# Performance work log

Measured on AMD Instinct MI355X. Metric: run time of the kernel, lower is better.

The kernel has to match this reference:

```python
import jax, jax.numpy as jnp
import numpy as np

INF = 100000000.0
TOPK = 13
ALPHA = 1
BETA = 6


def box_cxcywh_to_xyxy(b):
    cx, cy, w, h = jnp.split(b, 4, axis=-1)
    return jnp.concatenate([cx - 0.5 * w, cy - 0.5 * h, cx + 0.5 * w, cy + 0.5 * h], axis=-1)


def generalized_box_iou(boxes1, boxes2):
    # boxes1: [N,4] xyxy, boxes2: [G,4] xyxy -> [N,G]
    area1 = (boxes1[:, 2] - boxes1[:, 0]) * (boxes1[:, 3] - boxes1[:, 1])
    area2 = (boxes2[:, 2] - boxes2[:, 0]) * (boxes2[:, 3] - boxes2[:, 1])
    lt = jnp.maximum(boxes1[:, None, :2], boxes2[None, :, :2])
    rb = jnp.minimum(boxes1[:, None, 2:], boxes2[None, :, 2:])
    wh = jnp.clip(rb - lt, 0.0)
    inter = wh[..., 0] * wh[..., 1]
    union = area1[:, None] + area2[None, :] - inter
    iou = inter / union
    lt_e = jnp.minimum(boxes1[:, None, :2], boxes2[None, :, :2])
    rb_e = jnp.maximum(boxes1[:, None, 2:], boxes2[None, :, 2:])
    wh_e = jnp.clip(rb_e - lt_e, 0.0)
    area_e = wh_e[..., 0] * wh_e[..., 1]
    return iou - (area_e - union) / area_e


def _assign_one(cls_logits, bbox_pred, gt_boxes, gt_labels):
    # cls_logits [N,C], bbox_pred [N,4] cxcywh, gt_boxes [G,4] cxcywh, gt_labels [G]
    N = bbox_pred.shape[0]
    G = gt_boxes.shape[0]
    scores = jax.nn.sigmoid(cls_logits)
    overlaps = -generalized_box_iou(box_cxcywh_to_xyxy(bbox_pred), box_cxcywh_to_xyxy(gt_boxes))  # [N,G]
    bbox_scores = scores[:, gt_labels]                       # [N,G] gather per-gt class score
    alignment = bbox_scores ** ALPHA * overlaps ** BETA      # [N,G]
    # per-gt topk over queries
    cand_metrics, cand_idxs = jax.lax.top_k(alignment.T, TOPK)  # [G,K]
    is_pos = cand_metrics > 0
    vals = jnp.take_along_axis(overlaps.T, cand_idxs, axis=1)   # [G,K]
    rows = jnp.broadcast_to(jnp.arange(G)[:, None], (G, TOPK))
    cols = jnp.where(is_pos, cand_idxs, N)  # out-of-bounds col -> dropped
    oinf = jnp.full((G, N), -INF, dtype=overlaps.dtype)
    oinf = oinf.at[rows, cols].set(vals, mode='drop')
    max_overlaps = oinf.max(axis=0)     # [N]
    argmax_overlaps = oinf.argmax(axis=0)
    pos = max_overlaps != -INF
    assigned_gt_inds = jnp.where(pos, argmax_overlaps + 1, 0)
    assign_metrics = jnp.where(pos, alignment[jnp.arange(N), argmax_overlaps], 0.0)
    assigned_labels = jnp.where(pos, gt_labels[argmax_overlaps], -1)
    return assigned_gt_inds, assigned_labels, assign_metrics


def setup_inputs() -> dict:
    key = jax.random.key(0)
    k1, k2, k3, k4 = jax.random.split(key, 4)
    bs, N, C, G = 16, 4000, 80, 300
    return {
        'pred_logits': jax.random.normal(k1, (bs, N, C), dtype=jnp.float32),
        'pred_boxes': jax.random.uniform(k2, (bs, N, 4), dtype=jnp.float32, minval=0.05, maxval=0.95),
        'gt_boxes': jax.random.uniform(k3, (bs, G, 4), dtype=jnp.float32, minval=0.05, maxval=0.95),
        'gt_labels': jax.random.randint(k4, (bs, G), 0, C),
    }


def reference(pred_logits, pred_boxes, gt_boxes, gt_labels):
    # Fixed-shape equivalent of matched_list: assigned_gt_inds[b,q] == 0 means
    # background; k>0 means query q matched to gt k-1 (same semantics as the
    # (valid_query_idx, valid_assigned_gt_inds) pairs in the torch code).
    return jax.vmap(_assign_one)(pred_logits, pred_boxes, gt_boxes, gt_labels)
```

## Files before the change

### kernel.cpp

```cpp
#include <hip/hip_runtime.h>

#define NPRED  4000
#define NGROUP 1000
#define NGT    300
#define NCLS   80
#define TOPKK  13
#define NCHUNK 125

typedef unsigned long long u64;

__device__ __forceinline__ float frcp(float x) { return __builtin_amdgcn_rcpf(x); }
__device__ __forceinline__ float fexp(float x) {
    return __builtin_amdgcn_exp2f(x * 1.44269504088896341f);
}

__device__ __forceinline__ float neg_giou_pa(float4 p, float pa, float gx1, float gy1,
                                             float gx2, float gy2, float garea) {
    float whx = fmaxf(fminf(p.z, gx2) - fmaxf(p.x, gx1), 0.0f);
    float why = fmaxf(fminf(p.w, gy2) - fmaxf(p.y, gy1), 0.0f);
    float inter = whx * why;
    float uni = pa + garea - inter;
    float iou = inter * frcp(uni);
    float wex = fmaxf(p.z, gx2) - fminf(p.x, gx1);
    float wey = fmaxf(p.w, gy2) - fminf(p.y, gy1);
    float area_e = wex * wey;
    return (area_e - uni) * frcp(area_e) - iou;
}

__device__ __forceinline__ float4 to_xyxy(float4 pb) {
    return make_float4(pb.x - 0.5f * pb.z, pb.y - 0.5f * pb.w,
                       pb.x + 0.5f * pb.z, pb.y + 0.5f * pb.w);
}

__device__ __forceinline__ float sigmoid_fast(float x) {
    return frcp(1.0f + fexp(-x));
}

__device__ __forceinline__ float pow6(float x) {
    float x2 = x * x;
    float x4 = x2 * x2;
    return x2 * x4;
}

__device__ __forceinline__ unsigned ord_float(float f) {
    unsigned u = __float_as_uint(f);
    return u ^ ((unsigned)(((int)u) >> 31) | 0x80000000u);
}

__device__ __forceinline__ u64 pack_key(float v, int n) {
    return ((u64)__float_as_uint(v) << 32) | (u64)(~(unsigned)n);
}

__device__ __forceinline__ u64 wave_max_key(u64 b1) {
    float fv = __uint_as_float((unsigned)(b1 >> 32));
    float mv = fv;
    #pragma unroll
    for (int m = 1; m < 64; m <<= 1)
        mv = fmaxf(mv, __shfl_xor(mv, m, 64));
    u64 tied = __ballot(fv == mv);
    if ((tied & (tied - 1)) == 0ULL) {
        int src = __ffsll((unsigned long long)tied) - 1;
        return __shfl(b1, src, 64);
    }
    u64 t = b1;
    #pragma unroll
    for (int m = 1; m < 64; m <<= 1) {
        u64 o = __shfl_xor(t, m, 64);
        if (o > t) t = o;
    }
    return t;
}

__global__ void init_keys(u64* keys, int n) {
    int i = blockIdx.x * blockDim.x + threadIdx.x;
    if (i < n) keys[i] = 0ULL;
}

__global__ __launch_bounds__(256) void sig_transpose(const float* __restrict__ logits,
                                                     const float4* __restrict__ pboxes,
                                                     float* __restrict__ st,
                                                     float4* __restrict__ pxyxy,
                                                     float* __restrict__ parea,
                                                     u64* __restrict__ keys,
                                                     int total_keys) {
    const int tid = threadIdx.x;
    const int gid = blockIdx.x * 256 + tid;
    if (gid < total_keys) keys[gid] = 0ULL;

    const int b = blockIdx.x / NCHUNK;
    const int n0 = (blockIdx.x % NCHUNK) * 32;

    if (tid < 32) {
        int n = n0 + tid;
        float4 x = to_xyxy(pboxes[(size_t)b * NPRED + n]);
        pxyxy[(size_t)b * NPRED + n] = x;
        parea[(size_t)b * NPRED + n] = (x.z - x.x) * (x.w - x.y);
    }

    __shared__ float tile[NCLS][32 + 1];

    const float4* src = (const float4*)(logits + ((size_t)b * NPRED + n0) * NCLS);
    #pragma unroll
    for (int it = 0; it < 3; ++it) {
        int i4 = tid + it * 256;
        if (i4 < 640) {
            int p = i4 / 20;
            int c = (i4 - p * 20) * 4;
            float4 v = src[i4];
            tile[c + 0][p] = sigmoid_fast(v.x);
            tile[c + 1][p] = sigmoid_fast(v.y);
            tile[c + 2][p] = sigmoid_fast(v.z);
            tile[c + 3][p] = sigmoid_fast(v.w);
        }
    }
    __syncthreads();
    float* dstbase = st + (size_t)b * NCLS * NPRED + n0;
    #pragma unroll
    for (int it = 0; it < 3; ++it) {
        int w4 = tid + it * 256;
        if (w4 < 640) {
            int c = w4 >> 3, r4 = (w4 & 7) * 4;
            float4 v = make_float4(tile[c][r4], tile[c][r4 + 1],
                                   tile[c][r4 + 2], tile[c][r4 + 3]);
            *(float4*)(dstbase + (size_t)c * NPRED + r4) = v;
        }
    }
}

template <bool PRE>
__global__ __launch_bounds__(256) void topk_scatter(const float* __restrict__ logits,
                                                    const float* __restrict__ st,
                                                    const float4* __restrict__ pboxes,
                                                    const float4* __restrict__ pxyxy,
                                                    const float* __restrict__ parea,
                                                    const float4* __restrict__ gboxes,
                                                    const int* __restrict__ glabels,
                                                    u64* __restrict__ keys) {
    const int blk = blockIdx.x;
    const int b = blk / NGT;
    const int g = blk - b * NGT;
    const int tid = threadIdx.x;
    const int wave = tid >> 6;
    const int lane = tid & 63;

    __shared__ __align__(16) float s_key[NPRED];
    __shared__ u64 s_wave[4];
    __shared__ u64 s_win[TOPKK];

    float4 gb = gboxes[b * NGT + g];
    const int lab = glabels[b * NGT + g];
    const float gx1 = gb.x - 0.5f * gb.z;
    const float gy1 = gb.y - 0.5f * gb.w;
    const float gx2 = gb.x + 0.5f * gb.z;
    const float gy2 = gb.y + 0.5f * gb.w;
    const float garea = (gx2 - gx1) * (gy2 - gy1);

    const float* lg = logits + (size_t)b * NPRED * NCLS + lab;
    const float* srow = st + ((size_t)b * NCLS + lab) * NPRED;
    const float4* srow4 = (const float4*)srow;
    const float4* par4 = (const float4*)(parea + (size_t)b * NPRED);
    const float4* pbb = pboxes + (size_t)b * NPRED;
    const float4* pxr = pxyxy + (size_t)b * NPRED;

    float bv1 = -1.0f, bv2 = -1.0f;
    int   bn1 = 0,     bn2 = 0;
    #pragma unroll
    for (int j = 0; j < 4; ++j) {
        int grp = tid + j * 256;
        if (grp < NGROUP) {
            int n0 = grp * 4;
            float s0, s1, s2, s3;
            float4 p0, p1, p2, p3;
            float a0, a1, a2, a3;
            if (PRE) {
                float4 s4 = srow4[grp];
                s0 = s4.x; s1 = s4.y; s2 = s4.z; s3 = s4.w;
                float4 a4 = par4[grp];
                a0 = a4.x; a1 = a4.y; a2 = a4.z; a3 = a4.w;
                p0 = pxr[n0]; p1 = pxr[n0 + 1]; p2 = pxr[n0 + 2]; p3 = pxr[n0 + 3];
            } else {
                s0 = sigmoid_fast(lg[(size_t)(n0 + 0) * NCLS]);
                s1 = sigmoid_fast(lg[(size_t)(n0 + 1) * NCLS]);
                s2 = sigmoid_fast(lg[(size_t)(n0 + 2) * NCLS]);
                s3 = sigmoid_fast(lg[(size_t)(n0 + 3) * NCLS]);
                p0 = to_xyxy(pbb[n0]);     p1 = to_xyxy(pbb[n0 + 1]);
                p2 = to_xyxy(pbb[n0 + 2]); p3 = to_xyxy(pbb[n0 + 3]);
                a0 = (p0.z - p0.x) * (p0.w - p0.y);
                a1 = (p1.z - p1.x) * (p1.w - p1.y);
                a2 = (p2.z - p2.x) * (p2.w - p2.y);
                a3 = (p3.z - p3.x) * (p3.w - p3.y);
            }
            float v0 = s0 * pow6(neg_giou_pa(p0, a0, gx1, gy1, gx2, gy2, garea));
            float v1 = s1 * pow6(neg_giou_pa(p1, a1, gx1, gy1, gx2, gy2, garea));
            float v2 = s2 * pow6(neg_giou_pa(p2, a2, gx1, gy1, gx2, gy2, garea));
            float v3 = s3 * pow6(neg_giou_pa(p3, a3, gx1, gy1, gx2, gy2, garea));
            *(float4*)&s_key[n0] = make_float4(v0, v1, v2, v3);
            if (v0 > bv1) { bv2 = bv1; bn2 = bn1; bv1 = v0; bn1 = n0; }
            else if (v0 > bv2) { bv2 = v0; bn2 = n0; }
            if (v1 > bv1) { bv2 = bv1; bn2 = bn1; bv1 = v1; bn1 = n0 + 1; }
            else if (v1 > bv2) { bv2 = v1; bn2 = n0 + 1; }
            if (v2 > bv1) { bv2 = bv1; bn2 = bn1; bv1 = v2; bn1 = n0 + 2; }
            else if (v2 > bv2) { bv2 = v2; bn2 = n0 + 2; }
            if (v3 > bv1) { bv2 = bv1; bn2 = bn1; bv1 = v3; bn1 = n0 + 3; }
            else if (v3 > bv2) { bv2 = v3; bn2 = n0 + 3; }
        }
    }
    u64 b1 = pack_key(bv1, bn1);
    u64 b2 = pack_key(bv2, bn2);

    {
        u64 m1 = wave_max_key(b1);
        if (lane == 0) s_wave[wave] = m1;
    }

    int nwin = 0;
    for (int k = 0; k < TOPKK; ++k) {
        __syncthreads();
        u64 t1 = s_wave[0];
        u64 c;
        c = s_wave[1]; if (c > t1) t1 = c;
        c = s_wave[2]; if (c > t1) t1 = c;
        c = s_wave[3]; if (c > t1) t1 = c;
        if ((unsigned)(t1 >> 32) == 0u) break;
        if (tid == 0) s_win[k] = t1;
        nwin = k + 1;
        int n1 = (int)(~(unsigned)t1);
        int ownerTid = (n1 >> 2) & 255;
        if (tid == ownerTid) {
            s_key[n1] = 0.0f;
            if (b2 != 0ULL) { b1 = b2; b2 = 0ULL; }
            else {
                b1 = 0ULL;
                #pragma unroll
                for (int jj = 0; jj < 4; ++jj) {
                    int grp = tid + jj * 256;
                    if (grp >= NGROUP) continue;
                    int n0 = grp * 4;
                    float4 q = *(const float4*)&s_key[n0];
                    u64 c0 = pack_key(q.x, n0);
                    u64 c1 = pack_key(q.y, n0 + 1);
                    u64 c2 = pack_key(q.z, n0 + 2);
                    u64 c3 = pack_key(q.w, n0 + 3);
                    if (c0 > b1) { b2 = b1; b1 = c0; } else if (c0 > b2) b2 = c0;
                    if (c1 > b1) { b2 = b1; b1 = c1; } else if (c1 > b2) b2 = c1;
                    if (c2 > b1) { b2 = b1; b1 = c2; } else if (c2 > b2) b2 = c2;
                    if (c3 > b1) { b2 = b1; b1 = c3; } else if (c3 > b2) b2 = c3;
                }
            }
        }
        if ((ownerTid >> 6) == wave) {
            u64 m1 = wave_max_key(b1);
            if (lane == 0) s_wave[wave] = m1;
        }
    }
    __syncthreads();

    if (tid < nwin) {
        u64 t = s_win[tid];
        int wi = (int)(~(unsigned)t);
        float4 p;
        if (PRE) p = pxr[wi];
        else     p = to_xyxy(pbb[wi]);
        float pa = (p.z - p.x) * (p.w - p.y);
        float o = neg_giou_pa(p, pa, gx1, gy1, gx2, gy2, garea);
        unsigned mbits = (unsigned)(t >> 32) >> 16;
        u64 key = ((u64)ord_float(o) << 32)
                | ((u64)(511u - (unsigned)g) << 23)
                | ((u64)mbits << 7);
        atomicMax(&keys[(size_t)b * NPRED + wi], key);
    }
}

__global__ void finalize(const int* __restrict__ glabels,
                         const u64* __restrict__ keys,
                         float* __restrict__ out, int total) {
    int i = blockIdx.x * blockDim.x + threadIdx.x;
    if (i >= total) return;
    int b = i / NPRED;
    u64 key = keys[i];
    float o0 = 0.0f, o1 = -1.0f, o2 = 0.0f;
    if (key != 0ULL) {
        int g = 511 - (int)((key >> 23) & 0x1FF);
        o0 = (float)(g + 1);
        o1 = (float)glabels[b * NGT + g];
        o2 = __uint_as_float(((unsigned)(key >> 7) & 0xFFFFu) << 16);
    }
    out[i] = o0;
    out[(size_t)total + i] = o1;
    out[(size_t)2 * total + i] = o2;
}

extern "C" void kernel_launch(void* const* d_in, const int* in_sizes, int n_in,
                              void* d_out, int out_size, void* d_ws, size_t ws_size,
                              hipStream_t stream) {
    const float* logits  = (const float*)d_in[0];
    const float4* pboxes = (const float4*)d_in[1];
    const float4* gboxes = (const float4*)d_in[2];
    const int* glabels   = (const int*)d_in[3];

    const int bs = in_sizes[3] / NGT;
    const int total = bs * NPRED;
    char* ws = (char*)d_ws;
    u64* keys   = (u64*)ws;                    ws += (size_t)total * 8;
    float* st   = (float*)ws;                  ws += (size_t)bs * NCLS * NPRED * 4;
    float4* pxy = (float4*)ws;                 ws += (size_t)total * 16;
    float* par  = (float*)ws;                  ws += (size_t)total * 4;
    float* out = (float*)d_out;

    const size_t need = (size_t)(ws - (char*)d_ws);
    if (ws_size >= need) {
        sig_transpose<<<bs * NCHUNK, 256, 0, stream>>>(logits, pboxes, st, pxy,
                                                       par, keys, total);
        topk_scatter<true><<<bs * NGT, 256, 0, stream>>>(logits, st, pboxes, pxy,
                                                         par, gboxes, glabels, keys);
    } else {
        init_keys<<<(total + 255) / 256, 256, 0, stream>>>(keys, total);
        topk_scatter<false><<<bs * NGT, 256, 0, stream>>>(logits, st, pboxes, pxy,
                                                          par, gboxes, glabels, keys);
    }
    finalize<<<(total + 255) / 256, 256, 0, stream>>>(glabels, keys, out, total);
}
```

Measured before the change: 123.8 us.

## Process two ground-truth boxes per block and recompute instead of caching keys in LDS

Each topk_scatter block now handles a pair of GT boxes, so the pred box and area loads are shared between two alignment computations, and the grid is halved. The 16KB shared-memory key array is removed. When a thread's cached top-2 runs out, it recomputes its candidates through a noinline rescan function, using a bitmask to exclude entries already selected. This trades LDS footprint and per-box load traffic for extra barriers per top-k iteration, longer serial chains, and occasional recomputation.

```diff
diff --git a/kernel.cpp b/kernel.cpp
--- a/kernel.cpp
+++ b/kernel.cpp
@@ -3,6 +3,7 @@
 #define NPRED  4000
 #define NGROUP 1000
 #define NGT    300
+#define NGTH   150
 #define NCLS   80
 #define TOPKK  13
 #define NCHUNK 125
@@ -69,6 +70,55 @@
         if (o > t) t = o;
     }
     return t;
+}
+
+template <bool PRE>
+__device__ __attribute__((noinline)) void rescan_gt(
+        const float4* __restrict__ srow4, const float* __restrict__ lg,
+        const float4* __restrict__ par4, const float4* __restrict__ pxr,
+        const float4* __restrict__ pbb,
+        float gx1, float gy1, float gx2, float gy2, float garea,
+        int tid, unsigned mask, u64& r1, u64& r2) {
+    r1 = 0ULL; r2 = 0ULL;
+    for (int j = 0; j < 4; ++j) {
+        int grp = tid + j * 256;
+        if (grp >= NGROUP) continue;
+        int n0 = grp * 4;
+        float s0, s1, s2, s3;
+        float4 p0, p1, p2, p3;
+        float a0, a1, a2, a3;
+        if (PRE) {
+            float4 s4 = srow4[grp];
+            s0 = s4.x; s1 = s4.y; s2 = s4.z; s3 = s4.w;
+            float4 a4 = par4[grp];
+            a0 = a4.x; a1 = a4.y; a2 = a4.z; a3 = a4.w;
+            p0 = pxr[n0]; p1 = pxr[n0 + 1]; p2 = pxr[n0 + 2]; p3 = pxr[n0 + 3];
+        } else {
+            s0 = sigmoid_fast(lg[(size_t)(n0 + 0) * NCLS]);
+            s1 = sigmoid_fast(lg[(size_t)(n0 + 1) * NCLS]);
+            s2 = sigmoid_fast(lg[(size_t)(n0 + 2) * NCLS]);
+            s3 = sigmoid_fast(lg[(size_t)(n0 + 3) * NCLS]);
+            p0 = to_xyxy(pbb[n0]);     p1 = to_xyxy(pbb[n0 + 1]);
+            p2 = to_xyxy(pbb[n0 + 2]); p3 = to_xyxy(pbb[n0 + 3]);
+            a0 = (p0.z - p0.x) * (p0.w - p0.y);
+            a1 = (p1.z - p1.x) * (p1.w - p1.y);
+            a2 = (p2.z - p2.x) * (p2.w - p2.y);
+            a3 = (p3.z - p3.x) * (p3.w - p3.y);
+        }
+        float v0 = s0 * pow6(neg_giou_pa(p0, a0, gx1, gy1, gx2, gy2, garea));
+        float v1 = s1 * pow6(neg_giou_pa(p1, a1, gx1, gy1, gx2, gy2, garea));
+        float v2 = s2 * pow6(neg_giou_pa(p2, a2, gx1, gy1, gx2, gy2, garea));
+        float v3 = s3 * pow6(neg_giou_pa(p3, a3, gx1, gy1, gx2, gy2, garea));
+        unsigned mj = mask >> (j * 4);
+        if (!(mj & 1u)) { u64 c = pack_key(v0, n0);
+            if (c > r1) { r2 = r1; r1 = c; } else if (c > r2) r2 = c; }
+        if (!(mj & 2u)) { u64 c = pack_key(v1, n0 + 1);
+            if (c > r1) { r2 = r1; r1 = c; } else if (c > r2) r2 = c; }
+        if (!(mj & 4u)) { u64 c = pack_key(v2, n0 + 2);
+            if (c > r1) { r2 = r1; r1 = c; } else if (c > r2) r2 = c; }
+        if (!(mj & 8u)) { u64 c = pack_key(v3, n0 + 3);
+            if (c > r1) { r2 = r1; r1 = c; } else if (c > r2) r2 = c; }
+    }
 }
 
 __global__ void init_keys(u64* keys, int n) {
@@ -137,52 +187,62 @@
                                                     const int* __restrict__ glabels,
                                                     u64* __restrict__ keys) {
     const int blk = blockIdx.x;
-    const int b = blk / NGT;
-    const int g = blk - b * NGT;
+    const int b = blk / NGTH;
+    const int gp = blk - b * NGTH;
+    const int g0 = gp * 2, g1 = g0 + 1;
     const int tid = threadIdx.x;
     const int wave = tid >> 6;
     const int lane = tid & 63;
 
-    __shared__ __align__(16) float s_key[NPRED];
-    __shared__ u64 s_wave[4];
-    __shared__ u64 s_win[TOPKK];
-
-    float4 gb = gboxes[b * NGT + g];
-    const int lab = glabels[b * NGT + g];
-    const float gx1 = gb.x - 0.5f * gb.z;
-    const float gy1 = gb.y - 0.5f * gb.w;
-    const float gx2 = gb.x + 0.5f * gb.z;
-    const float gy2 = gb.y + 0.5f * gb.w;
-    const float garea = (gx2 - gx1) * (gy2 - gy1);
-
-    const float* lg = logits + (size_t)b * NPRED * NCLS + lab;
-    const float* srow = st + ((size_t)b * NCLS + lab) * NPRED;
-    const float4* srow4 = (const float4*)srow;
+    __shared__ u64 s_w0[4], s_w1[4];
+    __shared__ u64 s_win0[TOPKK], s_win1[TOPKK];
+
+    float4 gb0 = gboxes[b * NGT + g0];
+    float4 gb1 = gboxes[b * NGT + g1];
+    const int lab0 = glabels[b * NGT + g0];
+    const int lab1 = glabels[b * NGT + g1];
+    const float gx10 = gb0.x - 0.5f * gb0.z, gy10 = gb0.y - 0.5f * gb0.w;
+    const float gx20 = gb0.x + 0.5f * gb0.z, gy20 = gb0.y + 0.5f * gb0.w;
+    const float garea0 = (gx20 - gx10) * (gy20 - gy10);
+    const float gx11 = gb1.x - 0.5f * gb1.z, gy11 = gb1.y - 0.5f * gb1.w;
+    const float gx21 = gb1.x + 0.5f * gb1.z, gy21 = gb1.y + 0.5f * gb1.w;
+    const float garea1 = (gx21 - gx11) * (gy21 - gy11);
+
+    const float* lg0 = logits + (size_t)b * NPRED * NCLS + lab0;
+    const float* lg1 = logits + (size_t)b * NPRED * NCLS + lab1;
+    const float4* srow4_0 = (const float4*)(st + ((size_t)b * NCLS + lab0) * NPRED);
+    const float4* srow4_1 = (const float4*)(st + ((size_t)b * NCLS + lab1) * NPRED);
     const float4* par4 = (const float4*)(parea + (size_t)b * NPRED);
     const float4* pbb = pboxes + (size_t)b * NPRED;
     const float4* pxr = pxyxy + (size_t)b * NPRED;
 
-    float bv1 = -1.0f, bv2 = -1.0f;
-    int   bn1 = 0,     bn2 = 0;
+    float bv10 = -1.0f, bv20 = -1.0f;  int bn10 = 0, bn20 = 0;
+    float bv11 = -1.0f, bv21 = -1.0f;  int bn11 = 0, bn21 = 0;
     #pragma unroll
     for (int j = 0; j < 4; ++j) {
         int grp = tid + j * 256;
         if (grp < NGROUP) {
             int n0 = grp * 4;
-            float s0, s1, s2, s3;
+            float sa0, sa1, sa2, sa3, sb0, sb1, sb2, sb3;
             float4 p0, p1, p2, p3;
             float a0, a1, a2, a3;
             if (PRE) {
-                float4 s4 = srow4[grp];
-                s0 = s4.x; s1 = s4.y; s2 = s4.z; s3 = s4.w;
+                float4 s4a = srow4_0[grp];
+                sa0 = s4a.x; sa1 = s4a.y; sa2 = s4a.z; sa3 = s4a.w;
+                float4 s4b = srow4_1[grp];
+                sb0 = s4b.x; sb1 = s4b.y; sb2 = s4b.z; sb3 = s4b.w;
                 float4 a4 = par4[grp];
                 a0 = a4.x; a1 = a4.y; a2 = a4.z; a3 = a4.w;
                 p0 = pxr[n0]; p1 = pxr[n0 + 1]; p2 = pxr[n0 + 2]; p3 = pxr[n0 + 3];
             } else {
-                s0 = sigmoid_fast(lg[(size_t)(n0 + 0) * NCLS]);
-                s1 = sigmoid_fast(lg[(size_t)(n0 + 1) * NCLS]);
-                s2 = sigmoid_fast(lg[(size_t)(n0 + 2) * NCLS]);
-                s3 = sigmoid_fast(lg[(size_t)(n0 + 3) * NCLS]);
+                sa0 = sigmoid_fast(lg0[(size_t)(n0 + 0) * NCLS]);
+                sa1 = sigmoid_fast(lg0[(size_t)(n0 + 1) * NCLS]);
+                sa2 = sigmoid_fast(lg0[(size_t)(n0 + 2) * NCLS]);
+                sa3 = sigmoid_fast(lg0[(size_t)(n0 + 3) * NCLS]);
+                sb0 = sigmoid_fast(lg1[(size_t)(n0 + 0) * NCLS]);
+                sb1 = sigmoid_fast(lg1[(size_t)(n0 + 1) * NCLS]);
+                sb2 = sigmoid_fast(lg1[(size_t)(n0 + 2) * NCLS]);
+                sb3 = sigmoid_fast(lg1[(size_t)(n0 + 3) * NCLS]);
                 p0 = to_xyxy(pbb[n0]);     p1 = to_xyxy(pbb[n0 + 1]);
                 p2 = to_xyxy(pbb[n0 + 2]); p3 = to_xyxy(pbb[n0 + 3]);
                 a0 = (p0.z - p0.x) * (p0.w - p0.y);
@@ -190,82 +250,134 @@
                 a2 = (p2.z - p2.x) * (p2.w - p2.y);
                 a3 = (p3.z - p3.x) * (p3.w - p3.y);
             }
-            float v0 = s0 * pow6(neg_giou_pa(p0, a0, gx1, gy1, gx2, gy2, garea));
-            float v1 = s1 * pow6(neg_giou_pa(p1, a1, gx1, gy1, gx2, gy2, garea));
-            float v2 = s2 * pow6(neg_giou_pa(p2, a2, gx1, gy1, gx2, gy2, garea));
-            float v3 = s3 * pow6(neg_giou_pa(p3, a3, gx1, gy1, gx2, gy2, garea));
-            *(float4*)&s_key[n0] = make_float4(v0, v1, v2, v3);
-            if (v0 > bv1) { bv2 = bv1; bn2 = bn1; bv1 = v0; bn1 = n0; }
-            else if (v0 > bv2) { bv2 = v0; bn2 = n0; }
-            if (v1 > bv1) { bv2 = bv1; bn2 = bn1; bv1 = v1; bn1 = n0 + 1; }
-            else if (v1 > bv2) { bv2 = v1; bn2 = n0 + 1; }
-            if (v2 > bv1) { bv2 = bv1; bn2 = bn1; bv1 = v2; bn1 = n0 + 2; }
-            else if (v2 > bv2) { bv2 = v2; bn2 = n0 + 2; }
-            if (v3 > bv1) { bv2 = bv1; bn2 = bn1; bv1 = v3; bn1 = n0 + 3; }
-            else if (v3 > bv2) { bv2 = v3; bn2 = n0 + 3; }
-        }
-    }
-    u64 b1 = pack_key(bv1, bn1);
-    u64 b2 = pack_key(bv2, bn2);
+            {
+                float v0 = sa0 * pow6(neg_giou_pa(p0, a0, gx10, gy10, gx20, gy20, garea0));
+                float v1 = sa1 * pow6(neg_giou_pa(p1, a1, gx10, gy10, gx20, gy20, garea0));
+                float v2 = sa2 * pow6(neg_giou_pa(p2, a2, gx10, gy10, gx20, gy20, garea0));
+                float v3 = sa3 * pow6(neg_giou_pa(p3, a3, gx10, gy10, gx20, gy20, garea0));
+                if (v0 > bv10) { bv20 = bv10; bn20 = bn10; bv10 = v0; bn10 = n0; }
+                else if (v0 > bv20) { bv20 = v0; bn20 = n0; }
+                if (v1 > bv10) { bv20 = bv10; bn20 = bn10; bv10 = v1; bn10 = n0 + 1; }
+                else if (v1 > bv20) { bv20 = v1; bn20 = n0 + 1; }
+                if (v2 > bv10) { bv20 = bv10; bn20 = bn10; bv10 = v2; bn10 = n0 + 2; }
+                else if (v2 > bv20) { bv20 = v2; bn20 = n0 + 2; }
+                if (v3 > bv10) { bv20 = bv10; bn20 = bn10; bv10 = v3; bn10 = n0 + 3; }
+                else if (v3 > bv20) { bv20 = v3; bn20 = n0 + 3; }
+            }
+            {
+                float v0 = sb0 * pow6(neg_giou_pa(p0, a0, gx11, gy11, gx21, gy21, garea1));
+                float v1 = sb1 * pow6(neg_giou_pa(p1, a1, gx11, gy11, gx21, gy21, garea1));
+                float v2 = sb2 * pow6(neg_giou_pa(p2, a2, gx11, gy11, gx21, gy21, garea1));
+                float v3 = sb3 * pow6(neg_giou_pa(p3, a3, gx11, gy11, gx21, gy21, garea1));
+                if (v0 > bv11) { bv21 = bv11; bn21 = bn11; bv11 = v0; bn11 = n0; }
+                else if (v0 > bv21) { bv21 = v0; bn21 = n0; }
+                if (v1 > bv11) { bv21 = bv11; bn21 = bn11; bv11 = v1; bn11 = n0 + 1; }
+                else if (v1 > bv21) { bv21 = v1; bn21 = n0 + 1; }
+                if (v2 > bv11) { bv21 = bv11; bn21 = bn11; bv11 = v2; bn11 = n0 + 2; }
+                else if (v2 > bv21) { bv21 = v2; bn21 = n0 + 2; }
+                if (v3 > bv11) { bv21 = bv11; bn21 = bn11; bv11 = v3; bn11 = n0 + 3; }
+                else if (v3 > bv21) { bv21 = v3; bn21 = n0 + 3; }
+            }
+        }
+    }
+    u64 b1g0 = pack_key(bv10, bn10), b2g0 = pack_key(bv20, bn20);
+    u64 b1g1 = pack_key(bv11, bn11), b2g1 = pack_key(bv21, bn21);
+    unsigned mask0 = 0u, mask1 = 0u;
 
     {
-        u64 m1 = wave_max_key(b1);
-        if (lane == 0) s_wave[wave] = m1;
-    }
-
-    int nwin = 0;
+        u64 m = wave_max_key(b1g0);
+        if (lane == 0) s_w0[wave] = m;
+        m = wave_max_key(b1g1);
+        if (lane == 0) s_w1[wave] = m;
+    }
+
+    int nwin0 = 0, nwin1 = 0;
+    bool done0 = false, done1 = false;
     for (int k = 0; k < TOPKK; ++k) {
         __syncthreads();
-        u64 t1 = s_wave[0];
-        u64 c;
-        c = s_wave[1]; if (c > t1) t1 = c;
-        c = s_wave[2]; if (c > t1) t1 = c;
-        c = s_wave[3]; if (c > t1) t1 = c;
-        if ((unsigned)(t1 >> 32) == 0u) break;
-        if (tid == 0) s_win[k] = t1;
-        nwin = k + 1;
-        int n1 = (int)(~(unsigned)t1);
-        int ownerTid = (n1 >> 2) & 255;
-        if (tid == ownerTid) {
-            s_key[n1] = 0.0f;
-            if (b2 != 0ULL) { b1 = b2; b2 = 0ULL; }
+        if (!done0) {
+            u64 t = s_w0[0];
+            u64 c;
+            c = s_w0[1]; if (c > t) t = c;
+            c = s_w0[2]; if (c > t) t = c;
+            c = s_w0[3]; if (c > t) t = c;
+            if ((unsigned)(t >> 32) == 0u) done0 = true;
             else {
-                b1 = 0ULL;
-                #pragma unroll
-                for (int jj = 0; jj < 4; ++jj) {
-                    int grp = tid + jj * 256;
-                    if (grp >= NGROUP) continue;
-                    int n0 = grp * 4;
-                    float4 q = *(const float4*)&s_key[n0];
-                    u64 c0 = pack_key(q.x, n0);
-                    u64 c1 = pack_key(q.y, n0 + 1);
-                    u64 c2 = pack_key(q.z, n0 + 2);
-                    u64 c3 = pack_key(q.w, n0 + 3);
-                    if (c0 > b1) { b2 = b1; b1 = c0; } else if (c0 > b2) b2 = c0;
-                    if (c1 > b1) { b2 = b1; b1 = c1; } else if (c1 > b2) b2 = c1;
-                    if (c2 > b1) { b2 = b1; b1 = c2; } else if (c2 > b2) b2 = c2;
-                    if (c3 > b1) { b2 = b1; b1 = c3; } else if (c3 > b2) b2 = c3;
+                if (tid == 0) s_win0[k] = t;
+                nwin0 = k + 1;
+                if (k < TOPKK - 1) {
+                    int n1 = (int)(~(unsigned)t);
+                    int ownerTid = (n1 >> 2) & 255;
+                    if (tid == ownerTid) {
+                        mask0 |= 1u << (((n1 >> 10) << 2) | (n1 & 3));
+                        if (b2g0 != 0ULL) { b1g0 = b2g0; b2g0 = 0ULL; }
+                        else rescan_gt<PRE>(srow4_0, lg0, par4, pxr, pbb,
+                                            gx10, gy10, gx20, gy20, garea0,
+                                            tid, mask0, b1g0, b2g0);
+                    }
+                    if ((ownerTid >> 6) == wave) {
+                        u64 m = wave_max_key(b1g0);
+                        if (lane == 0) s_w0[wave] = m;
+                    }
                 }
             }
         }
-        if ((ownerTid >> 6) == wave) {
-            u64 m1 = wave_max_key(b1);
-            if (lane == 0) s_wave[wave] = m1;
-        }
+        __syncthreads();
+        if (!done1) {
+            u64 t = s_w1[0];
+            u64 c;
+            c = s_w1[1]; if (c > t) t = c;
+            c = s_w1[2]; if (c > t) t = c;
+            c = s_w1[3]; if (c > t) t = c;
+            if ((unsigned)(t >> 32) == 0u) done1 = true;
+            else {
+                if (tid == 0) s_win1[k] = t;
+                nwin1 = k + 1;
+                if (k < TOPKK - 1) {
+                    int n1 = (int)(~(unsigned)t);
+                    int ownerTid = (n1 >> 2) & 255;
+                    if (tid == ownerTid) {
+                        mask1 |= 1u << (((n1 >> 10) << 2) | (n1 & 3));
+                        if (b2g1 != 0ULL) { b1g1 = b2g1; b2g1 = 0ULL; }
+                        else rescan_gt<PRE>(srow4_1, lg1, par4, pxr, pbb,
+                                            gx11, gy11, gx21, gy21, garea1,
+                                            tid, mask1, b1g1, b2g1);
+                    }
+                    if ((ownerTid >> 6) == wave) {
+                        u64 m = wave_max_key(b1g1);
+                        if (lane == 0) s_w1[wave] = m;
+                    }
+                }
+            }
+        }
+        if (done0 && done1) break;
     }
     __syncthreads();
 
-    if (tid < nwin) {
-        u64 t = s_win[tid];
+    if (tid < nwin0) {
+        u64 t = s_win0[tid];
         int wi = (int)(~(unsigned)t);
         float4 p;
         if (PRE) p = pxr[wi];
         else     p = to_xyxy(pbb[wi]);
         float pa = (p.z - p.x) * (p.w - p.y);
-        float o = neg_giou_pa(p, pa, gx1, gy1, gx2, gy2, garea);
+        float o = neg_giou_pa(p, pa, gx10, gy10, gx20, gy20, garea0);
         unsigned mbits = (unsigned)(t >> 32) >> 16;
         u64 key = ((u64)ord_float(o) << 32)
-                | ((u64)(511u - (unsigned)g) << 23)
+                | ((u64)(511u - (unsigned)g0) << 23)
+                | ((u64)mbits << 7);
+        atomicMax(&keys[(size_t)b * NPRED + wi], key);
+    } else if (tid >= 64 && tid < 64 + nwin1) {
+        u64 t = s_win1[tid - 64];
+        int wi = (int)(~(unsigned)t);
+        float4 p;
+        if (PRE) p = pxr[wi];
+        else     p = to_xyxy(pbb[wi]);
+        float pa = (p.z - p.x) * (p.w - p.y);
+        float o = neg_giou_pa(p, pa, gx11, gy11, gx21, gy21, garea1);
+        unsigned mbits = (unsigned)(t >> 32) >> 16;
+        u64 key = ((u64)ord_float(o) << 32)
+                | ((u64)(511u - (unsigned)g1) << 23)
                 | ((u64)mbits << 7);
         atomicMax(&keys[(size_t)b * NPRED + wi], key);
     }
@@ -311,12 +423,12 @@
     if (ws_size >= need) {
         sig_transpose<<<bs * NCHUNK, 256, 0, stream>>>(logits, pboxes, st, pxy,
                                                        par, keys, total);
-        topk_scatter<true><<<bs * NGT, 256, 0, stream>>>(logits, st, pboxes, pxy,
-                                                         par, gboxes, glabels, keys);
+        topk_scatter<true><<<bs * NGTH, 256, 0, stream>>>(logits, st, pboxes, pxy,
+                                                          par, gboxes, glabels, keys);
     } else {
         init_keys<<<(total + 255) / 256, 256, 0, stream>>>(keys, total);
-        topk_scatter<false><<<bs * NGT, 256, 0, stream>>>(logits, st, pboxes, pxy,
-                                                          par, gboxes, glabels, keys);
+        topk_scatter<false><<<bs * NGTH, 256, 0, stream>>>(logits, st, pboxes, pxy,
+                                                           par, gboxes, glabels, keys);
     }
     finalize<<<(total + 255) / 256, 256, 0, stream>>>(glabels, keys, out, total);
 }
```

Result: slower. 164.7 us (+33.0%).
